# Kernel optimization log

Measured on AMD Instinct MI355X. Metric: run time of the kernel, lower is better.

Reference implementation:

```python
import jax, jax.numpy as jnp
import numpy as np

N = 50000      # nodes
E = 800000     # edges (avg degree 16)
F_IN = 128     # num_features
HID = 128      # hidden_channels
C = 40         # num_classes


def setup_inputs() -> dict:
    key = jax.random.key(0)
    ks = jax.random.split(key, 8)
    x = jax.random.normal(ks[0], (N, F_IN), dtype=jnp.float32)
    edge_index = jax.random.randint(ks[1], (2, E), 0, N, dtype=jnp.int64)
    def glorot(k, fan_in, fan_out):
        s = np.sqrt(6.0 / (fan_in + fan_out)).astype(np.float32)
        return jax.random.uniform(k, (fan_in, fan_out), jnp.float32, -s, s)
    return {
        "x": x,
        "W1": glorot(ks[2], F_IN, HID), "b1": jnp.zeros((HID,), jnp.float32),
        "W2": glorot(ks[3], HID, HID),  "b2": jnp.zeros((HID,), jnp.float32),
        "W3": glorot(ks[4], HID, C),   "b3": jnp.zeros((C,), jnp.float32),
        "edge_index": edge_index,
    }


def reference(x, W1, b1, W2, b2, W3, b3, edge_index):
    # GCN with symmetric normalization and self-loops (PyG GCNConv semantics),
    # eval mode (dropout p=0.0), log-softmax output.
    src = edge_index[0]
    dst = edge_index[1]
    loop = jnp.arange(N, dtype=edge_index.dtype)
    src = jnp.concatenate([src, loop])      # [E+N]
    dst = jnp.concatenate([dst, loop])      # [E+N]
    ew = jnp.ones((E + N,), jnp.float32)    # edge_weight=None -> ones
    # deg[i] = sum of incoming edge weights at node i (aggregation index = dst/col)
    deg = jax.ops.segment_sum(ew, dst, num_segments=N)
    dinv = jnp.where(deg > 0, jax.lax.rsqrt(deg), 0.0)
    norm = dinv[src] * ew * dinv[dst]       # [E+N]

    def conv(h, W, b):
        # linear transform first (no bias), then gather->scale->scatter-add, then bias
        m = (h @ W)[src] * norm[:, None]                      # [E+N, out]
        return jax.ops.segment_sum(m, dst, num_segments=N) + b

    h = jax.nn.relu(conv(x, W1, b1))
    h = jax.nn.relu(conv(h, W2, b2))
    h = conv(h, W3, b3)
    return jax.nn.log_softmax(h, axis=-1)
```

## Files before the change

### kernel.cpp

```cpp
#include <hip/hip_runtime.h>
#include <math.h>

#define N_NODES 50000
#define N_EDGES 800000
#define BUCKET 64
#define GEMM_BLKS 196
#define SCAT_BLKS 391

typedef __attribute__((ext_vector_type(8))) short short8;
typedef __attribute__((ext_vector_type(4))) float f32x4;

__device__ __forceinline__ ushort f2bf(float f) {
    union { float f; uint u; } v; v.f = f;
    uint r = v.u + 0x7FFFu + ((v.u >> 16) & 1u);
    return (ushort)(r >> 16);
}
__device__ __forceinline__ float bflo(uint p) {
    union { uint u; float f; } v; v.u = p << 16; return v.f;
}
__device__ __forceinline__ float bfhi(uint p) {
    union { uint u; float f; } v; v.u = p & 0xFFFF0000u; return v.f;
}

__global__ void dinv_k(const int* __restrict__ cnt, float* __restrict__ dinv) {
    int i = blockIdx.x * 256 + threadIdx.x;
    if (i < N_NODES) dinv[i] = rsqrtf((float)(cnt[i] + 1));
}

__global__ __launch_bounds__(512) void fused_gemm1_scatter_k(
        const float* __restrict__ Af, const float* __restrict__ W, ushort* __restrict__ Y,
        const int* __restrict__ src, const int* __restrict__ dst,
        int* __restrict__ cnt, int* __restrict__ colb) {
    constexpr int NT = 8;
    __shared__ ushort sB[4 * NT * 64 * 8];
    const int tid = threadIdx.x;

    if (blockIdx.x >= GEMM_BLKS) {
        const int t = (blockIdx.x - GEMM_BLKS) * 512 + tid;
        if (t >= N_EDGES / 4) return;
        const int4 s4 = reinterpret_cast<const int4*>(src)[t];
        const int4 d4 = reinterpret_cast<const int4*>(dst)[t];
        int p0 = atomicAdd(&cnt[d4.x], 1);
        int p1 = atomicAdd(&cnt[d4.y], 1);
        int p2 = atomicAdd(&cnt[d4.z], 1);
        int p3 = atomicAdd(&cnt[d4.w], 1);
        colb[(size_t)d4.x * BUCKET + p0] = s4.x;
        colb[(size_t)d4.y * BUCKET + p1] = s4.y;
        colb[(size_t)d4.z * BUCKET + p2] = s4.z;
        colb[(size_t)d4.w * BUCKET + p3] = s4.w;
        return;
    }

    constexpr int FP = NT * 16;
    for (int i = tid; i < 128 * FP; i += 512) {
        const int k = i / FP, n = i % FP;
        const int s = k >> 5, r2 = (k >> 3) & 3, j = k & 7;
        const int t = n >> 4, nl = n & 15;
        const int l = r2 * 16 + nl;
        const int lp = (l & 56) | ((l + (l >> 3)) & 7);
        sB[(((s * NT + t) * 64) + lp) * 8 + j] = f2bf(W[k * 128 + n]);
    }
    __syncthreads();

    const int wid = tid >> 6, lane = tid & 63;
    const int lp = (lane & 56) | ((lane + (lane >> 3)) & 7);
    const int t0 = blockIdx.x * 16 + wid * 2;
    const int t1 = t0 + 1;
    const int t0c = min(t0, N_NODES / 16 - 1);
    const int t1c = min(t1, N_NODES / 16 - 1);

    f32x4 acc[2][NT];
#pragma unroll
    for (int u = 0; u < 2; u++)
#pragma unroll
        for (int t = 0; t < NT; t++) acc[u][t] = (f32x4){0.f, 0.f, 0.f, 0.f};

#pragma unroll
    for (int s = 0; s < 4; s++) {
        short8 a0, a1;
        const int ko = 32 * s + 8 * (lane >> 4);
        const float4* p0 = reinterpret_cast<const float4*>(Af + (size_t)(t0c * 16 + (lane & 15)) * 128 + ko);
        const float4* p1 = reinterpret_cast<const float4*>(Af + (size_t)(t1c * 16 + (lane & 15)) * 128 + ko);
        float4 u0 = p0[0], u1 = p0[1], v0 = p1[0], v1 = p1[1];
        a0[0] = f2bf(u0.x); a0[1] = f2bf(u0.y); a0[2] = f2bf(u0.z); a0[3] = f2bf(u0.w);
        a0[4] = f2bf(u1.x); a0[5] = f2bf(u1.y); a0[6] = f2bf(u1.z); a0[7] = f2bf(u1.w);
        a1[0] = f2bf(v0.x); a1[1] = f2bf(v0.y); a1[2] = f2bf(v0.z); a1[3] = f2bf(v0.w);
        a1[4] = f2bf(v1.x); a1[5] = f2bf(v1.y); a1[6] = f2bf(v1.z); a1[7] = f2bf(v1.w);
#pragma unroll
        for (int t = 0; t < NT; t++) {
            short8 b = *reinterpret_cast<const short8*>(&sB[(((s * NT + t) * 64) + lp) * 8]);
            acc[0][t] = __builtin_amdgcn_mfma_f32_16x16x32_bf16(a0, b, acc[0][t], 0, 0, 0);
            acc[1][t] = __builtin_amdgcn_mfma_f32_16x16x32_bf16(a1, b, acc[1][t], 0, 0, 0);
        }
    }

    const int rl = 4 * (lane >> 4), cl = lane & 15;
#pragma unroll
    for (int u = 0; u < 2; u++) {
        const int tile = u ? t1 : t0;
        if (tile >= N_NODES / 16) continue;
        const int row0 = tile * 16;
#pragma unroll
        for (int t = 0; t < NT; t++) {
            const int c = 16 * t + cl;
#pragma unroll
            for (int g = 0; g < 4; g++)
                Y[(size_t)(row0 + rl + g) * 128 + c] = f2bf(acc[u][t][g]);
        }
    }
}

template <int NT>
__global__ __launch_bounds__(512) void gemm_mfma_k(const ushort* __restrict__ Ab,
                                                   const float* __restrict__ W,
                                                   ushort* __restrict__ Y,
                                                   const int fout) {
    __shared__ ushort sB[4 * NT * 64 * 8];
    const int tid = threadIdx.x;
    constexpr int FP = NT * 16;
    for (int i = tid; i < 128 * FP; i += 512) {
        const int k = i / FP, n = i % FP;
        const int s = k >> 5, r2 = (k >> 3) & 3, j = k & 7;
        const int t = n >> 4, nl = n & 15;
        const int l = r2 * 16 + nl;
        const int lp = (l & 56) | ((l + (l >> 3)) & 7);
        sB[(((s * NT + t) * 64) + lp) * 8 + j] = (n < fout) ? f2bf(W[k * fout + n]) : (ushort)0;
    }
    __syncthreads();

    const int wid = tid >> 6, lane = tid & 63;
    const int lp = (lane & 56) | ((lane + (lane >> 3)) & 7);
    const int t0 = blockIdx.x * 16 + wid * 2;
    const int t1 = t0 + 1;
    const int t0c = min(t0, N_NODES / 16 - 1);
    const int t1c = min(t1, N_NODES / 16 - 1);

    f32x4 acc[2][NT];
#pragma unroll
    for (int u = 0; u < 2; u++)
#pragma unroll
        for (int t = 0; t < NT; t++) acc[u][t] = (f32x4){0.f, 0.f, 0.f, 0.f};

#pragma unroll
    for (int s = 0; s < 4; s++) {
        const int ko = 32 * s + 8 * (lane >> 4);
        short8 a0 = *reinterpret_cast<const short8*>(Ab + (size_t)(t0c * 16 + (lane & 15)) * 128 + ko);
        short8 a1 = *reinterpret_cast<const short8*>(Ab + (size_t)(t1c * 16 + (lane & 15)) * 128 + ko);
#pragma unroll
        for (int t = 0; t < NT; t++) {
            short8 b = *reinterpret_cast<const short8*>(&sB[(((s * NT + t) * 64) + lp) * 8]);
            acc[0][t] = __builtin_amdgcn_mfma_f32_16x16x32_bf16(a0, b, acc[0][t], 0, 0, 0);
            acc[1][t] = __builtin_amdgcn_mfma_f32_16x16x32_bf16(a1, b, acc[1][t], 0, 0, 0);
        }
    }

    const int rl = 4 * (lane >> 4), cl = lane & 15;
#pragma unroll
    for (int u = 0; u < 2; u++) {
        const int tile = u ? t1 : t0;
        if (tile >= N_NODES / 16) continue;
        const int row0 = tile * 16;
#pragma unroll
        for (int t = 0; t < NT; t++) {
            const int c = 16 * t + cl;
            if (NT == 3 && c >= fout) continue;
#pragma unroll
            for (int g = 0; g < 4; g++)
                Y[(size_t)(row0 + rl + g) * fout + c] = f2bf(acc[u][t][g]);
        }
    }
}

template <bool RELU>
__global__ __launch_bounds__(256) void gather128_k(const ushort* __restrict__ XW,
                                                   const int* __restrict__ cnt,
                                                   const int* __restrict__ colb,
                                                   const float* __restrict__ dinv,
                                                   const float* __restrict__ bias,
                                                   ushort* __restrict__ out) {
    const int node = (blockIdx.x * 256 + threadIdx.x) >> 6;
    const int lane = threadIdx.x & 63;
    if (node >= N_NODES) return;
    const float di = dinv[node];
    const int n = cnt[node];
    const int4* bucket = reinterpret_cast<const int4*>(colb + (size_t)node * BUCKET);
    const uint* XW32 = reinterpret_cast<const uint*>(XW);

    float a0 = 0.f, a1 = 0.f, b0 = 0.f, b1 = 0.f;
    float c0 = 0.f, c1 = 0.f, d0 = 0.f, d1 = 0.f;
    int e = 0;
    for (; e + 4 <= n; e += 4) {
        const int4 s4 = bucket[e >> 2];
        const float w0 = dinv[s4.x] * di, w1 = dinv[s4.y] * di;
        const float w2 = dinv[s4.z] * di, w3 = dinv[s4.w] * di;
        const uint p0 = XW32[(size_t)s4.x * 64 + lane];
        const uint p1 = XW32[(size_t)s4.y * 64 + lane];
        const uint p2 = XW32[(size_t)s4.z * 64 + lane];
        const uint p3 = XW32[(size_t)s4.w * 64 + lane];
        a0 = fmaf(bflo(p0), w0, a0); a1 = fmaf(bfhi(p0), w0, a1);
        b0 = fmaf(bflo(p1), w1, b0); b1 = fmaf(bfhi(p1), w1, b1);
        c0 = fmaf(bflo(p2), w2, c0); c1 = fmaf(bfhi(p2), w2, c1);
        d0 = fmaf(bflo(p3), w3, d0); d1 = fmaf(bfhi(p3), w3, d1);
    }
    for (; e < n; e++) {
        const int s = colb[(size_t)node * BUCKET + e];
        const float w = dinv[s] * di;
        const uint p = XW32[(size_t)s * 64 + lane];
        a0 = fmaf(bflo(p), w, a0); a1 = fmaf(bfhi(p), w, a1);
    }
    const uint ps = XW32[(size_t)node * 64 + lane];
    const float ws = di * di;
    a0 = fmaf(bflo(ps), ws, (a0 + b0) + (c0 + d0)) + bias[2 * lane];
    a1 = fmaf(bfhi(ps), ws, (a1 + b1) + (c1 + d1)) + bias[2 * lane + 1];
    if (RELU) { a0 = fmaxf(a0, 0.f); a1 = fmaxf(a1, 0.f); }
    reinterpret_cast<uint*>(out)[(size_t)node * 64 + lane] =
        (uint)f2bf(a0) | ((uint)f2bf(a1) << 16);
}

__global__ __launch_bounds__(256) void gather40_lsm_k(const ushort* __restrict__ XW,
                                                      const int* __restrict__ cnt,
                                                      const int* __restrict__ colb,
                                                      const float* __restrict__ dinv,
                                                      const float* __restrict__ bias,
                                                      float* __restrict__ out) {
    const int node = (blockIdx.x * 256 + threadIdx.x) >> 6;
    const int lane = threadIdx.x & 63;
    if (node >= N_NODES) return;
    const int g = lane < 20 ? 0 : (lane < 40 ? 1 : 2);
    const int ll = lane - g * 20;
    const int llc = min(ll, 19);
    const float di = dinv[node];
    const int n = cnt[node];
    const uint* XW32 = reinterpret_cast<const uint*>(XW);

    float a0 = 0.f, a1 = 0.f;
    for (int e = g; e < n; e += 3) {
        const int s = colb[(size_t)node * BUCKET + e];
        const float w = dinv[s] * di;
        const uint p = XW32[(size_t)s * 20 + llc];
        a0 = fmaf(bflo(p), w, a0); a1 = fmaf(bfhi(p), w, a1);
    }
    const float t1 = __shfl(a0, lane + 20), t2 = __shfl(a0, lane + 40);
    const float u1 = __shfl(a1, lane + 20), u2 = __shfl(a1, lane + 40);
    float v0 = -INFINITY, v1 = -INFINITY;
    if (lane < 20) {
        const float s0 = a0 + t1 + t2, s1 = a1 + u1 + u2;
        const uint ps = XW32[(size_t)node * 20 + lane];
        const float ws = di * di;
        v0 = fmaf(bflo(ps), ws, s0) + bias[2 * lane];
        v1 = fmaf(bfhi(ps), ws, s1) + bias[2 * lane + 1];
    }
    float m = fmaxf(v0, v1);
#pragma unroll
    for (int o = 32; o > 0; o >>= 1) m = fmaxf(m, __shfl_xor(m, o));
    float s = (lane < 20) ? (expf(v0 - m) + expf(v1 - m)) : 0.f;
#pragma unroll
    for (int o = 32; o > 0; o >>= 1) s += __shfl_xor(s, o);
    if (lane < 20) {
        const float ls = m + logf(s);
        float2 r; r.x = v0 - ls; r.y = v1 - ls;
        reinterpret_cast<float2*>(out)[(size_t)node * 20 + lane] = r;
    }
}

extern "C" void kernel_launch(void* const* d_in, const int* in_sizes, int n_in,
                              void* d_out, int out_size, void* d_ws, size_t ws_size,
                              hipStream_t stream) {
    const float* x  = (const float*)d_in[0];
    const float* W1 = (const float*)d_in[1];
    const float* b1 = (const float*)d_in[2];
    const float* W2 = (const float*)d_in[3];
    const float* b2 = (const float*)d_in[4];
    const float* W3 = (const float*)d_in[5];
    const float* b3 = (const float*)d_in[6];
    const int* ei   = (const int*)d_in[7];
    const int* srcp = ei;
    const int* dstp = ei + N_EDGES;
    float* out = (float*)d_out;

    int*    cnt  = (int*)d_ws;
    float*  dinv = (float*)(cnt + 50176);
    int*    colb = (int*)(dinv + 50176);
    ushort* B0   = (ushort*)(colb + (size_t)N_NODES * BUCKET);
    ushort* B1   = B0 + (size_t)N_NODES * 128;

    const int NB_N = (N_NODES + 255) / 256;
    const int NB_W = (N_NODES * 64) / 256;

    hipMemsetAsync(cnt, 0, 50176 * sizeof(int), stream);
    fused_gemm1_scatter_k<<<GEMM_BLKS + SCAT_BLKS, 512, 0, stream>>>(
        x, W1, B1, srcp, dstp, cnt, colb);
    dinv_k<<<NB_N, 256, 0, stream>>>(cnt, dinv);

    gather128_k<true><<<NB_W, 256, 0, stream>>>(B1, cnt, colb, dinv, b1, B0);
    gemm_mfma_k<8><<<GEMM_BLKS, 512, 0, stream>>>(B0, W2, B1, 128);
    gather128_k<true><<<NB_W, 256, 0, stream>>>(B1, cnt, colb, dinv, b2, B0);
    gemm_mfma_k<3><<<GEMM_BLKS, 512, 0, stream>>>(B0, W3, B1, 40);
    gather40_lsm_k<<<NB_W, 256, 0, stream>>>(B1, cnt, colb, dinv, b3, out);
}
```

Baseline: 275.2 us.

## Fuse gather-aggregation into following GEMM, use 16-bit neighbor indices, inline dinv

Each gather128 pass is merged with the next layer's MFMA GEMM. A block aggregates 32 nodes into shared memory and then multiplies them by W, so the intermediate activation buffer is never written to or read from global memory. Neighbor buckets are stored as ushort to halve index traffic, and the dinv kernel is dropped in favour of recomputing rsqrt(cnt+1) inline. The scatter blocks each handle 8 edges and are scheduled before the GEMM blocks. The cost is extra rsqrt work and extra cnt reads per edge. The ushort indices also only hold node ids below 65536, which N=50000 happens to satisfy.

Measured after the change: 287.5 us. 4.5% more time.

```diff
diff --git a/kernel.cpp b/kernel.cpp
--- a/kernel.cpp
+++ b/kernel.cpp
@@ -4,8 +4,8 @@
 #define N_NODES 50000
 #define N_EDGES 800000
 #define BUCKET 64
+#define SCAT_BLKS 196
 #define GEMM_BLKS 196
-#define SCAT_BLKS 391
 
 typedef __attribute__((ext_vector_type(8))) short short8;
 typedef __attribute__((ext_vector_type(4))) float f32x4;
@@ -22,32 +22,37 @@
     union { uint u; float f; } v; v.u = p & 0xFFFF0000u; return v.f;
 }
 
-__global__ void dinv_k(const int* __restrict__ cnt, float* __restrict__ dinv) {
-    int i = blockIdx.x * 256 + threadIdx.x;
-    if (i < N_NODES) dinv[i] = rsqrtf((float)(cnt[i] + 1));
-}
-
 __global__ __launch_bounds__(512) void fused_gemm1_scatter_k(
         const float* __restrict__ Af, const float* __restrict__ W, ushort* __restrict__ Y,
         const int* __restrict__ src, const int* __restrict__ dst,
-        int* __restrict__ cnt, int* __restrict__ colb) {
+        int* __restrict__ cnt, ushort* __restrict__ colb) {
     constexpr int NT = 8;
     __shared__ ushort sB[4 * NT * 64 * 8];
     const int tid = threadIdx.x;
 
-    if (blockIdx.x >= GEMM_BLKS) {
-        const int t = (blockIdx.x - GEMM_BLKS) * 512 + tid;
-        if (t >= N_EDGES / 4) return;
-        const int4 s4 = reinterpret_cast<const int4*>(src)[t];
-        const int4 d4 = reinterpret_cast<const int4*>(dst)[t];
-        int p0 = atomicAdd(&cnt[d4.x], 1);
-        int p1 = atomicAdd(&cnt[d4.y], 1);
-        int p2 = atomicAdd(&cnt[d4.z], 1);
-        int p3 = atomicAdd(&cnt[d4.w], 1);
-        colb[(size_t)d4.x * BUCKET + p0] = s4.x;
-        colb[(size_t)d4.y * BUCKET + p1] = s4.y;
-        colb[(size_t)d4.z * BUCKET + p2] = s4.z;
-        colb[(size_t)d4.w * BUCKET + p3] = s4.w;
+    if (blockIdx.x < SCAT_BLKS) {
+        const int t = blockIdx.x * 512 + tid;
+        if (t >= N_EDGES / 8) return;
+        const int4* s32 = reinterpret_cast<const int4*>(src);
+        const int4* d32 = reinterpret_cast<const int4*>(dst);
+        const int4 sa = s32[2 * t], sb = s32[2 * t + 1];
+        const int4 da = d32[2 * t], db = d32[2 * t + 1];
+        int p0 = atomicAdd(&cnt[da.x], 1);
+        int p1 = atomicAdd(&cnt[da.y], 1);
+        int p2 = atomicAdd(&cnt[da.z], 1);
+        int p3 = atomicAdd(&cnt[da.w], 1);
+        int p4 = atomicAdd(&cnt[db.x], 1);
+        int p5 = atomicAdd(&cnt[db.y], 1);
+        int p6 = atomicAdd(&cnt[db.z], 1);
+        int p7 = atomicAdd(&cnt[db.w], 1);
+        colb[(size_t)da.x * BUCKET + p0] = (ushort)sa.x;
+        colb[(size_t)da.y * BUCKET + p1] = (ushort)sa.y;
+        colb[(size_t)da.z * BUCKET + p2] = (ushort)sa.z;
+        colb[(size_t)da.w * BUCKET + p3] = (ushort)sa.w;
+        colb[(size_t)db.x * BUCKET + p4] = (ushort)sb.x;
+        colb[(size_t)db.y * BUCKET + p5] = (ushort)sb.y;
+        colb[(size_t)db.z * BUCKET + p6] = (ushort)sb.z;
+        colb[(size_t)db.w * BUCKET + p7] = (ushort)sb.w;
         return;
     }
 
@@ -64,7 +69,7 @@
 
     const int wid = tid >> 6, lane = tid & 63;
     const int lp = (lane & 56) | ((lane + (lane >> 3)) & 7);
-    const int t0 = blockIdx.x * 16 + wid * 2;
+    const int t0 = (blockIdx.x - SCAT_BLKS) * 16 + wid * 2;
     const int t1 = t0 + 1;
     const int t0c = min(t0, N_NODES / 16 - 1);
     const int t1c = min(t1, N_NODES / 16 - 1);
@@ -111,116 +116,110 @@
 }
 
 template <int NT>
-__global__ __launch_bounds__(512) void gemm_mfma_k(const ushort* __restrict__ Ab,
-                                                   const float* __restrict__ W,
-                                                   ushort* __restrict__ Y,
-                                                   const int fout) {
+__global__ __launch_bounds__(512) void gathergemm_k(const ushort* __restrict__ XW,
+                                                    const int* __restrict__ cnt,
+                                                    const ushort* __restrict__ colb,
+                                                    const float* __restrict__ bias,
+                                                    const float* __restrict__ W,
+                                                    ushort* __restrict__ Y,
+                                                    const int fout) {
     __shared__ ushort sB[4 * NT * 64 * 8];
+    __shared__ uint sA[32 * 64];
     const int tid = threadIdx.x;
+    const int wid = tid >> 6, lane = tid & 63;
+
     constexpr int FP = NT * 16;
     for (int i = tid; i < 128 * FP; i += 512) {
         const int k = i / FP, n = i % FP;
         const int s = k >> 5, r2 = (k >> 3) & 3, j = k & 7;
         const int t = n >> 4, nl = n & 15;
         const int l = r2 * 16 + nl;
-        const int lp = (l & 56) | ((l + (l >> 3)) & 7);
-        sB[(((s * NT + t) * 64) + lp) * 8 + j] = (n < fout) ? f2bf(W[k * fout + n]) : (ushort)0;
+        const int lpw = (l & 56) | ((l + (l >> 3)) & 7);
+        sB[(((s * NT + t) * 64) + lpw) * 8 + j] = (n < fout) ? f2bf(W[k * fout + n]) : (ushort)0;
+    }
+
+    const int row0 = blockIdx.x * 32;
+    const uint* XW32 = reinterpret_cast<const uint*>(XW);
+#pragma unroll
+    for (int u = 0; u < 4; u++) {
+        const int r = wid * 4 + u;
+        const int node = min(row0 + r, N_NODES - 1);
+        const int n = cnt[node];
+        const float di = rsqrtf((float)(n + 1));
+        const ushort4* bucket = reinterpret_cast<const ushort4*>(colb + (size_t)node * BUCKET);
+
+        float a0 = 0.f, a1 = 0.f, b0 = 0.f, b1 = 0.f;
+        float c0 = 0.f, c1 = 0.f, d0 = 0.f, d1 = 0.f;
+        int e = 0;
+        for (; e + 4 <= n; e += 4) {
+            const ushort4 s4 = bucket[e >> 2];
+            const float w0 = rsqrtf((float)(cnt[s4.x] + 1)) * di;
+            const float w1 = rsqrtf((float)(cnt[s4.y] + 1)) * di;
+            const float w2 = rsqrtf((float)(cnt[s4.z] + 1)) * di;
+            const float w3 = rsqrtf((float)(cnt[s4.w] + 1)) * di;
+            const uint p0 = XW32[(size_t)s4.x * 64 + lane];
+            const uint p1 = XW32[(size_t)s4.y * 64 + lane];
+            const uint p2 = XW32[(size_t)s4.z * 64 + lane];
+            const uint p3 = XW32[(size_t)s4.w * 64 + lane];
+            a0 = fmaf(bflo(p0), w0, a0); a1 = fmaf(bfhi(p0), w0, a1);
+            b0 = fmaf(bflo(p1), w1, b0); b1 = fmaf(bfhi(p1), w1, b1);
+            c0 = fmaf(bflo(p2), w2, c0); c1 = fmaf(bfhi(p2), w2, c1);
+            d0 = fmaf(bflo(p3), w3, d0); d1 = fmaf(bfhi(p3), w3, d1);
+        }
+        for (; e < n; e++) {
+            const ushort s = colb[(size_t)node * BUCKET + e];
+            const float w = rsqrtf((float)(cnt[s] + 1)) * di;
+            const uint p = XW32[(size_t)s * 64 + lane];
+            a0 = fmaf(bflo(p), w, a0); a1 = fmaf(bfhi(p), w, a1);
+        }
+        const uint ps = XW32[(size_t)node * 64 + lane];
+        const float ws = di * di;
+        a0 = fmaxf(fmaf(bflo(ps), ws, (a0 + b0) + (c0 + d0)) + bias[2 * lane], 0.f);
+        a1 = fmaxf(fmaf(bfhi(ps), ws, (a1 + b1) + (c1 + d1)) + bias[2 * lane + 1], 0.f);
+        sA[r * 64 + (lane ^ ((r & 7) << 2))] = (uint)f2bf(a0) | ((uint)f2bf(a1) << 16);
     }
     __syncthreads();
 
-    const int wid = tid >> 6, lane = tid & 63;
+    if (NT == 3 && wid >= 6) return;
+    const int tile = wid & 1;
+    const int ar = tile * 16 + (lane & 15);
+    const int hi = lane >> 4;
     const int lp = (lane & 56) | ((lane + (lane >> 3)) & 7);
-    const int t0 = blockIdx.x * 16 + wid * 2;
-    const int t1 = t0 + 1;
-    const int t0c = min(t0, N_NODES / 16 - 1);
-    const int t1c = min(t1, N_NODES / 16 - 1);
-
-    f32x4 acc[2][NT];
-#pragma unroll
-    for (int u = 0; u < 2; u++)
-#pragma unroll
-        for (int t = 0; t < NT; t++) acc[u][t] = (f32x4){0.f, 0.f, 0.f, 0.f};
+    constexpr int UPW = (NT == 8) ? 2 : 1;
+
+    f32x4 acc[UPW];
+#pragma unroll
+    for (int i = 0; i < UPW; i++) acc[i] = (f32x4){0.f, 0.f, 0.f, 0.f};
 
 #pragma unroll
     for (int s = 0; s < 4; s++) {
-        const int ko = 32 * s + 8 * (lane >> 4);
-        short8 a0 = *reinterpret_cast<const short8*>(Ab + (size_t)(t0c * 16 + (lane & 15)) * 128 + ko);
-        short8 a1 = *reinterpret_cast<const short8*>(Ab + (size_t)(t1c * 16 + (lane & 15)) * 128 + ko);
-#pragma unroll
-        for (int t = 0; t < NT; t++) {
+        short8 a = *reinterpret_cast<const short8*>(
+            &sA[ar * 64 + ((16 * s + 4 * hi) ^ ((ar & 7) << 2))]);
+#pragma unroll
+        for (int i = 0; i < UPW; i++) {
+            const int t = (wid >> 1) + i * 4;
             short8 b = *reinterpret_cast<const short8*>(&sB[(((s * NT + t) * 64) + lp) * 8]);
-            acc[0][t] = __builtin_amdgcn_mfma_f32_16x16x32_bf16(a0, b, acc[0][t], 0, 0, 0);
-            acc[1][t] = __builtin_amdgcn_mfma_f32_16x16x32_bf16(a1, b, acc[1][t], 0, 0, 0);
-        }
-    }
-
-    const int rl = 4 * (lane >> 4), cl = lane & 15;
-#pragma unroll
-    for (int u = 0; u < 2; u++) {
-        const int tile = u ? t1 : t0;
-        if (tile >= N_NODES / 16) continue;
-        const int row0 = tile * 16;
-#pragma unroll
-        for (int t = 0; t < NT; t++) {
-            const int c = 16 * t + cl;
-            if (NT == 3 && c >= fout) continue;
-#pragma unroll
-            for (int g = 0; g < 4; g++)
-                Y[(size_t)(row0 + rl + g) * fout + c] = f2bf(acc[u][t][g]);
-        }
-    }
-}
-
-template <bool RELU>
-__global__ __launch_bounds__(256) void gather128_k(const ushort* __restrict__ XW,
-                                                   const int* __restrict__ cnt,
-                                                   const int* __restrict__ colb,
-                                                   const float* __restrict__ dinv,
-                                                   const float* __restrict__ bias,
-                                                   ushort* __restrict__ out) {
-    const int node = (blockIdx.x * 256 + threadIdx.x) >> 6;
-    const int lane = threadIdx.x & 63;
-    if (node >= N_NODES) return;
-    const float di = dinv[node];
-    const int n = cnt[node];
-    const int4* bucket = reinterpret_cast<const int4*>(colb + (size_t)node * BUCKET);
-    const uint* XW32 = reinterpret_cast<const uint*>(XW);
-
-    float a0 = 0.f, a1 = 0.f, b0 = 0.f, b1 = 0.f;
-    float c0 = 0.f, c1 = 0.f, d0 = 0.f, d1 = 0.f;
-    int e = 0;
-    for (; e + 4 <= n; e += 4) {
-        const int4 s4 = bucket[e >> 2];
-        const float w0 = dinv[s4.x] * di, w1 = dinv[s4.y] * di;
-        const float w2 = dinv[s4.z] * di, w3 = dinv[s4.w] * di;
-        const uint p0 = XW32[(size_t)s4.x * 64 + lane];
-        const uint p1 = XW32[(size_t)s4.y * 64 + lane];
-        const uint p2 = XW32[(size_t)s4.z * 64 + lane];
-        const uint p3 = XW32[(size_t)s4.w * 64 + lane];
-        a0 = fmaf(bflo(p0), w0, a0); a1 = fmaf(bfhi(p0), w0, a1);
-        b0 = fmaf(bflo(p1), w1, b0); b1 = fmaf(bfhi(p1), w1, b1);
-        c0 = fmaf(bflo(p2), w2, c0); c1 = fmaf(bfhi(p2), w2, c1);
-        d0 = fmaf(bflo(p3), w3, d0); d1 = fmaf(bfhi(p3), w3, d1);
-    }
-    for (; e < n; e++) {
-        const int s = colb[(size_t)node * BUCKET + e];
-        const float w = dinv[s] * di;
-        const uint p = XW32[(size_t)s * 64 + lane];
-        a0 = fmaf(bflo(p), w, a0); a1 = fmaf(bfhi(p), w, a1);
-    }
-    const uint ps = XW32[(size_t)node * 64 + lane];
-    const float ws = di * di;
-    a0 = fmaf(bflo(ps), ws, (a0 + b0) + (c0 + d0)) + bias[2 * lane];
-    a1 = fmaf(bfhi(ps), ws, (a1 + b1) + (c1 + d1)) + bias[2 * lane + 1];
-    if (RELU) { a0 = fmaxf(a0, 0.f); a1 = fmaxf(a1, 0.f); }
-    reinterpret_cast<uint*>(out)[(size_t)node * 64 + lane] =
-        (uint)f2bf(a0) | ((uint)f2bf(a1) << 16);
+            acc[i] = __builtin_amdgcn_mfma_f32_16x16x32_bf16(a, b, acc[i], 0, 0, 0);
+        }
+    }
+
+    const int rl = 4 * hi, cl = lane & 15;
+#pragma unroll
+    for (int i = 0; i < UPW; i++) {
+        const int t = (wid >> 1) + i * 4;
+        const int c = 16 * t + cl;
+        if (c >= fout) continue;
+#pragma unroll
+        for (int g = 0; g < 4; g++) {
+            const int row = row0 + tile * 16 + rl + g;
+            if (row < N_NODES) Y[(size_t)row * fout + c] = f2bf(acc[i][g]);
+        }
+    }
 }
 
 __global__ __launch_bounds__(256) void gather40_lsm_k(const ushort* __restrict__ XW,
                                                       const int* __restrict__ cnt,
-                                                      const int* __restrict__ colb,
-                                                      const float* __restrict__ dinv,
+                                                      const ushort* __restrict__ colb,
                                                       const float* __restrict__ bias,
                                                       float* __restrict__ out) {
     const int node = (blockIdx.x * 256 + threadIdx.x) >> 6;
@@ -229,14 +228,14 @@
     const int g = lane < 20 ? 0 : (lane < 40 ? 1 : 2);
     const int ll = lane - g * 20;
     const int llc = min(ll, 19);
-    const float di = dinv[node];
     const int n = cnt[node];
+    const float di = rsqrtf((float)(n + 1));
     const uint* XW32 = reinterpret_cast<const uint*>(XW);
 
     float a0 = 0.f, a1 = 0.f;
     for (int e = g; e < n; e += 3) {
-        const int s = colb[(size_t)node * BUCKET + e];
-        const float w = dinv[s] * di;
+        const ushort s = colb[(size_t)node * BUCKET + e];
+        const float w = rsqrtf((float)(cnt[s] + 1)) * di;
         const uint p = XW32[(size_t)s * 20 + llc];
         a0 = fmaf(bflo(p), w, a0); a1 = fmaf(bfhi(p), w, a1);
     }
@@ -279,22 +278,17 @@
     float* out = (float*)d_out;
 
     int*    cnt  = (int*)d_ws;
-    float*  dinv = (float*)(cnt + 50176);
-    int*    colb = (int*)(dinv + 50176);
-    ushort* B0   = (ushort*)(colb + (size_t)N_NODES * BUCKET);
+    ushort* colb = (ushort*)(cnt + 50176);
+    ushort* B0   = colb + (size_t)N_NODES * BUCKET;
     ushort* B1   = B0 + (size_t)N_NODES * 128;
 
-    const int NB_N = (N_NODES + 255) / 256;
     const int NB_W = (N_NODES * 64) / 256;
+    const int NB_GG = (N_NODES + 31) / 32;
 
     hipMemsetAsync(cnt, 0, 50176 * sizeof(int), stream);
-    fused_gemm1_scatter_k<<<GEMM_BLKS + SCAT_BLKS, 512, 0, stream>>>(
+    fused_gemm1_scatter_k<<<SCAT_BLKS + GEMM_BLKS, 512, 0, stream>>>(
         x, W1, B1, srcp, dstp, cnt, colb);
-    dinv_k<<<NB_N, 256, 0, stream>>>(cnt, dinv);
-
-    gather128_k<true><<<NB_W, 256, 0, stream>>>(B1, cnt, colb, dinv, b1, B0);
-    gemm_mfma_k<8><<<GEMM_BLKS, 512, 0, stream>>>(B0, W2, B1, 128);
-    gather128_k<true><<<NB_W, 256, 0, stream>>>(B1, cnt, colb, dinv, b2, B0);
-    gemm_mfma_k<3><<<GEMM_BLKS, 512, 0, stream>>>(B0, W3, B1, 40);
-    gather40_lsm_k<<<NB_W, 256, 0, stream>>>(B1, cnt, colb, dinv, b3, out);
-}
+    gathergemm_k<8><<<NB_GG, 512, 0, stream>>>(B1, cnt, colb, b1, W2, B0, 128);
+    gathergemm_k<3><<<NB_GG, 512, 0, stream>>>(B0, cnt, colb, b2, W3, B1, 40);
+    gather40_lsm_k<<<NB_W, 256, 0, stream>>>(B1, cnt, colb, b3, out);
+}
```
